# Optimization experiments

Measured on AMD Instinct MI355X. Metric: run time of the kernel, lower is better.

## Reference

```python
import jax, jax.numpy as jnp
import numpy as np
import math

B, S, D, H = 2048, 32, 1024, 16
DK = D // H
EPS = 1e-5

def setup_inputs() -> dict:
    key = jax.random.key(0)
    ks = jax.random.split(key, 8)
    w_scale = 0.02  # realistic init scale for linear weights
    # Weights stored as (d_in, d_out): y = x @ W + b (same math as torch x @ W.T)
    return {
        "x":  jax.random.normal(ks[0], (B, S, D), jnp.float32),
        "ln_g": jnp.ones((D,), jnp.float32),
        "ln_b": jnp.zeros((D,), jnp.float32),
        "wq": jax.random.normal(ks[1], (D, D), jnp.float32) * w_scale,
        "bq": jnp.zeros((D,), jnp.float32),
        "wk": jax.random.normal(ks[2], (D, D), jnp.float32) * w_scale,
        "bk": jnp.zeros((D,), jnp.float32),
        "wv": jax.random.normal(ks[3], (D, D), jnp.float32) * w_scale,
        "bv": jnp.zeros((D,), jnp.float32),
        "wo": jax.random.normal(ks[4], (D, D), jnp.float32) * w_scale,
        "bo": jnp.zeros((D,), jnp.float32),
        "rel_bias": jax.random.normal(ks[5], (H, 32, 32), jnp.float32),
    }

def reference(x, ln_g, ln_b, wq, bq, wk, bk, wv, bv, wo, bo, rel_bias):
    b, s, d = x.shape
    h = rel_bias.shape[0]
    dk = d // h
    residual = x
    # LayerNorm (eps=1e-5)
    mu = jnp.mean(x, axis=-1, keepdims=True)
    var = jnp.mean(jnp.square(x - mu), axis=-1, keepdims=True)
    xn = (x - mu) * jax.lax.rsqrt(var + EPS) * ln_g + ln_b
    # QKV projections -> [b, h, s, dk]
    def split_heads(t):
        return t.reshape(b, s, h, dk).transpose(0, 2, 1, 3)
    Q = split_heads(xn @ wq + bq)
    K = split_heads(xn @ wk + bk)
    V = split_heads(xn @ wv + bv)
    scores = jnp.einsum('bhqd,bhkd->bhqk', Q, K) / jnp.sqrt(jnp.float32(dk))
    if s <= 32:  # static at trace time, matching the torch branch
        scores = scores + rel_bias[:, :s, :s][None]
    attn = jax.nn.softmax(scores, axis=-1)
    ctx = jnp.einsum('bhqk,bhkd->bhqd', attn, V)
    ctx = ctx.transpose(0, 2, 1, 3).reshape(b, s, d)
    out = ctx @ wo + bo  # dropout is identity in eval
    return residual + out
```

## Files before the change

kernel.cpp:

```cpp
#include <hip/hip_runtime.h>
#include <stdint.h>


typedef __attribute__((ext_vector_type(8))) short bf16x8;
typedef __attribute__((ext_vector_type(4))) float f32x4;
typedef __attribute__((ext_vector_type(16))) float f32x16;

__device__ __forceinline__ float bf2f(unsigned short u) {
    return __uint_as_float(((unsigned)u) << 16);
}
__device__ __forceinline__ unsigned short f2bf(float f) {
    unsigned u = __float_as_uint(f);
    u += 0x7FFFu + ((u >> 16) & 1u);
    return (unsigned short)(u >> 16);
}
__device__ __forceinline__ uint4 pack8(const float* f) {
    uint4 u;
    u.x = (unsigned)f2bf(f[0]) | ((unsigned)f2bf(f[1]) << 16);
    u.y = (unsigned)f2bf(f[2]) | ((unsigned)f2bf(f[3]) << 16);
    u.z = (unsigned)f2bf(f[4]) | ((unsigned)f2bf(f[5]) << 16);
    u.w = (unsigned)f2bf(f[6]) | ((unsigned)f2bf(f[7]) << 16);
    return u;
}

typedef __attribute__((address_space(3))) unsigned lds_u32;
typedef const __attribute__((address_space(1))) unsigned glb_u32;
__device__ __forceinline__ void gld16(const void* g, void* l) {
    __builtin_amdgcn_global_load_lds((glb_u32*)g, (lds_u32*)l, 16, 0, 0);
}

__global__ __launch_bounds__(256) void transpose_w(
    const float* __restrict__ wq, const float* __restrict__ wk,
    const float* __restrict__ wv, const float* __restrict__ wo,
    unsigned short* __restrict__ wcatT, unsigned short* __restrict__ woT)
{
    __shared__ unsigned short T[64 * 72];
    int bid = blockIdx.x;
    int p = bid >> 8;
    int t = bid & 255;
    int k0 = (t >> 4) * 64, n0 = (t & 15) * 64;
    const float* src = (p == 0) ? wq : (p == 1) ? wk : (p == 2) ? wv : wo;
    unsigned short* dst = (p < 3) ? (wcatT + (size_t)p * 1048576) : woT;
    int tid = threadIdx.x;
#pragma unroll
    for (int it = 0; it < 2; it++) {
        int flat = it * 2048 + tid * 8;
        int r = flat >> 6, c = flat & 63;
        const float* s4 = src + (size_t)(k0 + r) * 1024 + n0 + c;
        float4 u0 = *(const float4*)s4;
        float4 u1 = *(const float4*)(s4 + 4);
        float f[8] = {u0.x, u0.y, u0.z, u0.w, u1.x, u1.y, u1.z, u1.w};
        *(uint4*)&T[r * 72 + c] = pack8(f);
    }
    __syncthreads();
#pragma unroll
    for (int it = 0; it < 2; it++) {
        int flat = it * 2048 + tid * 8;
        int rn = flat >> 6, ck = flat & 63;
        unsigned short v[8];
#pragma unroll
        for (int j = 0; j < 8; j++) v[j] = T[(ck + j) * 72 + rn];
        uint4 u;
        u.x = (unsigned)v[0] | ((unsigned)v[1] << 16);
        u.y = (unsigned)v[2] | ((unsigned)v[3] << 16);
        u.z = (unsigned)v[4] | ((unsigned)v[5] << 16);
        u.w = (unsigned)v[6] | ((unsigned)v[7] << 16);
        *(uint4*)(dst + (size_t)(n0 + rn) * 1024 + k0 + ck) = u;
    }
}

__global__ __launch_bounds__(256) void ln_kernel(
    const float* __restrict__ x, const float* __restrict__ gg,
    const float* __restrict__ bb, unsigned short* __restrict__ xn)
{
    int l = threadIdx.x & 63;
    size_t row = (size_t)blockIdx.x * 4 + (threadIdx.x >> 6);
    const float* xr = x + row * 1024;
    float f0[8], f1[8];
    *(float4*)&f0[0] = *(const float4*)(xr + l * 8);
    *(float4*)&f0[4] = *(const float4*)(xr + l * 8 + 4);
    *(float4*)&f1[0] = *(const float4*)(xr + 512 + l * 8);
    *(float4*)&f1[4] = *(const float4*)(xr + 512 + l * 8 + 4);
    float s = 0.f, s2 = 0.f;
#pragma unroll
    for (int j = 0; j < 8; j++) { s += f0[j] + f1[j]; s2 += f0[j] * f0[j] + f1[j] * f1[j]; }
#pragma unroll
    for (int m = 1; m < 64; m <<= 1) { s += __shfl_xor(s, m); s2 += __shfl_xor(s2, m); }
    float mu = s * (1.f / 1024.f);
    float var = s2 * (1.f / 1024.f) - mu * mu;
    float rs = rsqrtf(var + 1e-5f);
    float fg0[8], fg1[8], fb0[8], fb1[8];
    *(float4*)&fg0[0] = *(const float4*)(gg + l * 8);
    *(float4*)&fg0[4] = *(const float4*)(gg + l * 8 + 4);
    *(float4*)&fg1[0] = *(const float4*)(gg + 512 + l * 8);
    *(float4*)&fg1[4] = *(const float4*)(gg + 512 + l * 8 + 4);
    *(float4*)&fb0[0] = *(const float4*)(bb + l * 8);
    *(float4*)&fb0[4] = *(const float4*)(bb + l * 8 + 4);
    *(float4*)&fb1[0] = *(const float4*)(bb + 512 + l * 8);
    *(float4*)&fb1[4] = *(const float4*)(bb + 512 + l * 8 + 4);
    float o0[8], o1[8];
#pragma unroll
    for (int j = 0; j < 8; j++) {
        o0[j] = (f0[j] - mu) * rs * fg0[j] + fb0[j];
        o1[j] = (f1[j] - mu) * rs * fg1[j] + fb1[j];
    }
    *(uint4*)(xn + row * 1024 + l * 8) = pack8(o0);
    *(uint4*)(xn + row * 1024 + 512 + l * 8) = pack8(o1);
}

#define FENCE asm volatile("" ::: "memory")
#define BARRIER do { FENCE; __builtin_amdgcn_s_barrier(); FENCE; } while (0)
#define WAIT_LGKM0 do { asm volatile("s_waitcnt lgkmcnt(0)" ::: "memory"); \
                        __builtin_amdgcn_sched_barrier(0); } while (0)
#define VMCNT(n) asm volatile("s_waitcnt vmcnt(" #n ")" ::: "memory")

#define FQ_SA(buf) (LDSU + (buf) * 8192)
#define FQ_SB(buf) (LDSU + 16384 + (buf) * 12288)
#define QS_OFF 0
#define KS_OFF 9216
#define VT_OFF 18432
#define PS_OFF 28672

#define ASTG(buf, g, koff) gld16(Ag + (size_t)(g) * 32768 + (koff), \
                                 FQ_SA(buf) + ((g) * 32 + w * 8) * 64)
#define BSTG(buf, p, c, koff) gld16(((p) == 0 ? Bgq : (p) == 1 ? Bgk : Bgv) + (size_t)(c) * 32768 + (koff), \
                                    FQ_SB(buf) + ((p) * 64 + (c) * 32 + w * 8) * 64)

#define FLDA(buf, q, ks) (*(const bf16x8*)&FQ_SA(buf)[ \
    (wm * 64 + (q) * 16 + (l & 15)) * 64 + ((((ks) * 32) + khi) ^ aswz)])
#define FLDB(buf, cf, ks) (*(const bf16x8*)&FQ_SB(buf)[ \
    (wn * 96 + (cf) * 16 + (l & 15)) * 64 + ((((ks) * 32) + khi) ^ aswz)])

#define MFMA_HEX(q) do { \
    _Pragma("unroll") \
    for (int cf = 0; cf < 6; cf++) { \
        acc[q][cf] = __builtin_amdgcn_mfma_f32_16x16x32_bf16(aF0, bF[cf][0], acc[q][cf], 0, 0, 0); \
        acc[q][cf] = __builtin_amdgcn_mfma_f32_16x16x32_bf16(aF1, bF[cf][1], acc[q][cf], 0, 0, 0); \
    } } while (0)

#define FPHASE(buf, q, STAGE_STMT, TAIL_STMT) do { \
    bf16x8 aF0 = FLDA(buf, q, 0), aF1 = FLDA(buf, q, 1); \
    if ((q) == 0) { \
        _Pragma("unroll") \
        for (int cf = 0; cf < 6; cf++) { bF[cf][0] = FLDB(buf, cf, 0); bF[cf][1] = FLDB(buf, cf, 1); } \
    } \
    STAGE_STMT; \
    BARRIER; \
    WAIT_LGKM0; \
    __builtin_amdgcn_s_setprio(1); \
    MFMA_HEX(q); \
    __builtin_amdgcn_s_setprio(0); \
    TAIL_STMT; \
    BARRIER; \
} while (0)

__global__ __launch_bounds__(256, 2) void fqa2_kernel(
    const unsigned short* __restrict__ A, const unsigned short* __restrict__ wcatT,
    const float* __restrict__ bq, const float* __restrict__ bk,
    const float* __restrict__ bv, const float* __restrict__ rb,
    unsigned short* __restrict__ ctx)
{
    __shared__ __align__(16) unsigned short LDSU[40960];
    int cpx = gridDim.x >> 3;
    int bid = (blockIdx.x & 7) * cpx + (blockIdx.x >> 3);
    int mp = bid >> 4, h = bid & 15;
    int m0 = mp * 128;
    int tid = threadIdx.x, l = tid & 63, w = tid >> 6;
    int wm = w >> 1, wn = w & 1;
    int khi = (l >> 4) * 8;
    int aswz = (l & 7) * 8;
    int swzc = ((l & 7) ^ (l >> 3)) * 8;

    const unsigned short* Ag  = A + (size_t)(m0 + w * 8 + (l >> 3)) * 1024 + swzc;
    const unsigned short* Bgq = wcatT + (size_t)(h * 64 + w * 8 + (l >> 3)) * 1024 + swzc;
    const unsigned short* Bgk = Bgq + 1048576ull;
    const unsigned short* Bgv = Bgq + 2097152ull;

    f32x4 acc[4][6];
#pragma unroll
    for (int i = 0; i < 4; i++)
#pragma unroll
        for (int j = 0; j < 6; j++)
#pragma unroll
            for (int v = 0; v < 4; v++) acc[i][j][v] = 0.f;

    bf16x8 bF[6][2];

    ASTG(0, 0, 0); ASTG(0, 1, 0); ASTG(0, 2, 0); ASTG(0, 3, 0);
    BSTG(0, 0, 0, 0); BSTG(0, 0, 1, 0); BSTG(0, 1, 0, 0);
    BSTG(0, 1, 1, 0); BSTG(0, 2, 0, 0); BSTG(0, 2, 1, 0);
    BSTG(1, 0, 0, 64); BSTG(1, 0, 1, 64); BSTG(1, 1, 0, 64);
    BSTG(1, 1, 1, 64); BSTG(1, 2, 0, 64); BSTG(1, 2, 1, 64);
    VMCNT(6);
    BARRIER;

    for (int it = 0; it < 7; ++it) {
        int ko1 = (2 * it + 1) * 64, ko2 = (2 * it + 2) * 64, ko3 = (2 * it + 3) * 64;
        FPHASE(0, 0, do { ASTG(1, 0, ko1); ASTG(1, 1, ko1); } while (0), (void)0);
        FPHASE(0, 1, do { ASTG(1, 2, ko1); ASTG(1, 3, ko1); } while (0), (void)0);
        FPHASE(0, 2, do { BSTG(0, 0, 0, ko2); BSTG(0, 0, 1, ko2); BSTG(0, 1, 0, ko2); } while (0), (void)0);
        FPHASE(0, 3, do { BSTG(0, 1, 1, ko2); BSTG(0, 2, 0, ko2); BSTG(0, 2, 1, ko2); } while (0), VMCNT(6));
        FPHASE(1, 0, do { ASTG(0, 0, ko2); ASTG(0, 1, ko2); } while (0), (void)0);
        FPHASE(1, 1, do { ASTG(0, 2, ko2); ASTG(0, 3, ko2); } while (0), (void)0);
        FPHASE(1, 2, do { BSTG(1, 0, 0, ko3); BSTG(1, 0, 1, ko3); BSTG(1, 1, 0, ko3); } while (0), (void)0);
        FPHASE(1, 3, do { BSTG(1, 1, 1, ko3); BSTG(1, 2, 0, ko3); BSTG(1, 2, 1, ko3); } while (0), VMCNT(6));
    }
    FPHASE(0, 0, do { ASTG(1, 0, 960); ASTG(1, 1, 960); } while (0), (void)0);
    FPHASE(0, 1, do { ASTG(1, 2, 960); ASTG(1, 3, 960); } while (0), (void)0);
    FPHASE(0, 2, (void)0, (void)0);
    FPHASE(0, 3, (void)0, VMCNT(0));
    FPHASE(1, 0, (void)0, (void)0);
    FPHASE(1, 1, (void)0, (void)0);
    FPHASE(1, 2, (void)0, (void)0);
    FPHASE(1, 3, (void)0, (void)0);
    __builtin_amdgcn_sched_barrier(0);

#pragma unroll
    for (int cf = 0; cf < 6; cf++) {
        int colg = wn * 96 + cf * 16 + (l & 15);
        int seg = colg >> 6;
        int cseg = colg & 63;
        const float* bp = (seg == 0) ? bq : (seg == 1) ? bk : bv;
        float bias = bp[h * 64 + cseg];
#pragma unroll
        for (int ai = 0; ai < 4; ai++) {
#pragma unroll
            for (int v = 0; v < 4; v++) {
                int row = wm * 64 + ai * 16 + (l >> 4) * 4 + v;
                unsigned short val = f2bf(acc[ai][cf][v] + bias);
                if (seg == 0)      LDSU[QS_OFF + row * 72 + cseg] = val;
                else if (seg == 1) LDSU[KS_OFF + row * 72 + cseg] = val;
                else               LDSU[VT_OFF + (((row >> 5) << 6) + cseg) * 40 + (row & 31)] = val;
            }
        }
    }
    __syncthreads();

    {
        int col = l & 31, hi = l >> 5;
        f32x16 s;
#pragma unroll
        for (int i = 0; i < 16; i++) s[i] = 0.f;
#pragma unroll
        for (int t = 0; t < 4; t++) {
            bf16x8 aQ = *(const bf16x8*)&LDSU[QS_OFF + (w * 32 + col) * 72 + t * 16 + hi * 8];
            bf16x8 bK = *(const bf16x8*)&LDSU[KS_OFF + (w * 32 + col) * 72 + t * 16 + hi * 8];
            s = __builtin_amdgcn_mfma_f32_32x32x16_bf16(aQ, bK, s, 0, 0, 0);
        }
        const float* rbh = rb + h * 1024;
        unsigned short* ps = LDSU + PS_OFF + w * 1280;
#pragma unroll
        for (int r = 0; r < 16; r++) {
            int m = (r & 3) + 8 * (r >> 2) + 4 * hi;
            float v = s[r] * 0.125f + rbh[m * 32 + col];
            float mx = v;
#pragma unroll
            for (int msk = 1; msk < 32; msk <<= 1) mx = fmaxf(mx, __shfl_xor(mx, msk));
            float e = __expf(v - mx);
            float sm = e;
#pragma unroll
            for (int msk = 1; msk < 32; msk <<= 1) sm += __shfl_xor(sm, msk);
            ps[m * 40 + col] = f2bf(e / sm);
        }
        bf16x8 pa0 = *(const bf16x8*)&ps[col * 40 + hi * 8];
        bf16x8 pa1 = *(const bf16x8*)&ps[col * 40 + 16 + hi * 8];
        size_t rowb = ((size_t)mp * 4 + w) * 32;
#pragma unroll
        for (int c2 = 0; c2 < 2; c2++) {
            bf16x8 vb0 = *(const bf16x8*)&LDSU[VT_OFF + (w * 64 + c2 * 32 + col) * 40 + hi * 8];
            bf16x8 vb1 = *(const bf16x8*)&LDSU[VT_OFF + (w * 64 + c2 * 32 + col) * 40 + 16 + hi * 8];
            f32x16 o;
#pragma unroll
            for (int i = 0; i < 16; i++) o[i] = 0.f;
            o = __builtin_amdgcn_mfma_f32_32x32x16_bf16(pa0, vb0, o, 0, 0, 0);
            o = __builtin_amdgcn_mfma_f32_32x32x16_bf16(pa1, vb1, o, 0, 0, 0);
#pragma unroll
            for (int r = 0; r < 16; r++) {
                int m = (r & 3) + 8 * (r >> 2) + 4 * hi;
                ctx[(rowb + m) * 1024 + h * 64 + c2 * 32 + col] = f2bf(o[r]);
            }
        }
    }
}

#define SAp(buf) (LDSB + (buf) * 16384)
#define SBp(buf) (LDSB + 32768 + (buf) * 16384)

#define STG(gb, hh, kcol, ldsreg) do { \
    const unsigned short* _g = (gb) + (size_t)((hh) * 128) * 1024 + (kcol); \
    unsigned short* _d = (ldsreg) + ((hh) * 128 + w * 8) * 64; \
    gld16(_g, _d); gld16(_g + 64 * 1024, _d + 64 * 64); } while (0)

#define LDA(buf, q, rfq, ks) (*(const bf16x8*)&SAp(buf)[ \
    (wm * 128 + (q) * 32 + (rfq) * 16 + (l & 15)) * 64 + ((((ks) * 32) + khi) ^ aswz)])
#define LDB(buf, cf, ks) (*(const bf16x8*)&SBp(buf)[ \
    (wn * 64 + (cf) * 16 + (l & 15)) * 64 + ((((ks) * 32) + khi) ^ aswz)])

#define MFMA_QUAD(q) do { \
    _Pragma("unroll") \
    for (int cf = 0; cf < 4; cf++) { \
        acc[(q)*2+0][cf] = __builtin_amdgcn_mfma_f32_16x16x32_bf16(aF00, bF[cf][0], acc[(q)*2+0][cf], 0, 0, 0); \
        acc[(q)*2+0][cf] = __builtin_amdgcn_mfma_f32_16x16x32_bf16(aF01, bF[cf][1], acc[(q)*2+0][cf], 0, 0, 0); \
        acc[(q)*2+1][cf] = __builtin_amdgcn_mfma_f32_16x16x32_bf16(aF10, bF[cf][0], acc[(q)*2+1][cf], 0, 0, 0); \
        acc[(q)*2+1][cf] = __builtin_amdgcn_mfma_f32_16x16x32_bf16(aF11, bF[cf][1], acc[(q)*2+1][cf], 0, 0, 0); \
    } } while (0)

#define PHASE(buf, q, STAGE_STMT, TAIL_STMT) do { \
    bf16x8 aF00 = LDA(buf, q, 0, 0), aF01 = LDA(buf, q, 0, 1); \
    bf16x8 aF10 = LDA(buf, q, 1, 0), aF11 = LDA(buf, q, 1, 1); \
    if ((q) == 0) { \
        _Pragma("unroll") \
        for (int cf = 0; cf < 4; cf++) { bF[cf][0] = LDB(buf, cf, 0); bF[cf][1] = LDB(buf, cf, 1); } \
    } \
    STAGE_STMT; \
    BARRIER; \
    WAIT_LGKM0; \
    __builtin_amdgcn_s_setprio(1); \
    MFMA_QUAD(q); \
    __builtin_amdgcn_s_setprio(0); \
    TAIL_STMT; \
    BARRIER; \
} while (0)

__global__ __launch_bounds__(512, 2) void gemm8res(
    const unsigned short* __restrict__ A, const unsigned short* __restrict__ Bt,
    const float* __restrict__ bz0, const float* __restrict__ resid,
    float* __restrict__ out, int NTL)
{
    __shared__ __align__(16) unsigned short LDSB[65536];
    int cpx = gridDim.x >> 3;
    int bid = (blockIdx.x & 7) * cpx + (blockIdx.x >> 3);
    int mt = bid / NTL, ntl = bid % NTL;
    int m0 = mt * 256, n0 = ntl * 256;
    int tid = threadIdx.x, l = tid & 63, w = tid >> 6;
    int wm = w >> 2, wn = w & 3;
    int khi = (l >> 4) * 8;
    int aswz = (l & 7) * 8;

    const unsigned short* Ag = A + (size_t)(m0 + w * 8 + (l >> 3)) * 1024 + ((l & 7) ^ (l >> 3)) * 8;
    const unsigned short* Bg = Bt + (size_t)(n0 + w * 8 + (l >> 3)) * 1024 + ((l & 7) ^ (l >> 3)) * 8;
    unsigned short* sA0 = SAp(0);
    unsigned short* sA1 = SAp(1);
    unsigned short* sB0 = SBp(0);
    unsigned short* sB1 = SBp(1);

    f32x4 acc[8][4];
#pragma unroll
    for (int i = 0; i < 8; i++)
#pragma unroll
        for (int j = 0; j < 4; j++)
#pragma unroll
            for (int v = 0; v < 4; v++) acc[i][j][v] = 0.f;

    bf16x8 bF[4][2];

    STG(Ag, 0, 0, sA0); STG(Ag, 1, 0, sA0);
    STG(Bg, 0, 0, sB0); STG(Bg, 1, 0, sB0);
    STG(Bg, 0, 64, sB1); STG(Bg, 1, 64, sB1);
    VMCNT(4);
    BARRIER;

    for (int it = 0; it < 7; ++it) {
        int koff = it * 128;
        PHASE(0, 0, STG(Ag, 0, koff + 64, sA1), (void)0);
        PHASE(0, 1, STG(Ag, 1, koff + 64, sA1), (void)0);
        PHASE(0, 2, STG(Bg, 0, koff + 128, sB0), (void)0);
        PHASE(0, 3, STG(Bg, 1, koff + 128, sB0), VMCNT(4));
        PHASE(1, 0, STG(Ag, 0, koff + 128, sA0), (void)0);
        PHASE(1, 1, STG(Ag, 1, koff + 128, sA0), (void)0);
        PHASE(1, 2, STG(Bg, 0, koff + 192, sB1), (void)0);
        PHASE(1, 3, STG(Bg, 1, koff + 192, sB1), VMCNT(4));
    }
    PHASE(0, 0, STG(Ag, 0, 960, sA1), (void)0);
    PHASE(0, 1, STG(Ag, 1, 960, sA1), (void)0);
    PHASE(0, 2, (void)0, (void)0);
    PHASE(0, 3, (void)0, VMCNT(0));
    PHASE(1, 0, (void)0, (void)0);
    PHASE(1, 1, (void)0, (void)0);
    PHASE(1, 2, (void)0, (void)0);
    PHASE(1, 3, (void)0, (void)0);
    __builtin_amdgcn_sched_barrier(0);

    float* Cf = (float*)LDSB;
    int gcol = n0 + l * 4;
    float4 bzv = *(const float4*)(bz0 + gcol);
#pragma unroll
    for (int pass = 0; pass < 2; pass++) {
        __syncthreads();
#pragma unroll
        for (int rfq = 0; rfq < 4; rfq++) {
            int rf = pass * 4 + rfq;
#pragma unroll
            for (int cf = 0; cf < 4; cf++) {
                int c0 = wn * 64 + cf * 16 + (l & 15);
                int c4 = c0 >> 2, ce = c0 & 3;
#pragma unroll
                for (int v = 0; v < 4; v++) {
                    int rl = wm * 64 + rfq * 16 + (l >> 4) * 4 + v;
                    Cf[rl * 256 + ((c4 ^ (rl & 7)) << 2) + ce] = acc[rf][cf][v];
                }
            }
        }
        __syncthreads();
#pragma unroll
        for (int rb4 = 0; rb4 < 4; rb4++) {
            float4 rz[4], cv[4];
#pragma unroll
            for (int k = 0; k < 4; k++) {
                int rr = (rb4 * 4 + k) * 8 + w;
                int grow = m0 + (rr & 63) + ((rr >> 6) << 7) + pass * 64;
                rz[k] = *(const float4*)(resid + (size_t)grow * 1024 + gcol);
            }
#pragma unroll
            for (int k = 0; k < 4; k++) {
                int rr = (rb4 * 4 + k) * 8 + w;
                cv[k] = *(const float4*)&Cf[rr * 256 + ((l ^ (rr & 7)) << 2)];
            }
#pragma unroll
            for (int k = 0; k < 4; k++) {
                int rr = (rb4 * 4 + k) * 8 + w;
                int grow = m0 + (rr & 63) + ((rr >> 6) << 7) + pass * 64;
                float4 o;
                o.x = cv[k].x + bzv.x + rz[k].x;
                o.y = cv[k].y + bzv.y + rz[k].y;
                o.z = cv[k].z + bzv.z + rz[k].z;
                o.w = cv[k].w + bzv.w + rz[k].w;
                *(float4*)(out + (size_t)grow * 1024 + gcol) = o;
            }
        }
    }
}

extern "C" void kernel_launch(void* const* d_in, const int* in_sizes, int n_in,
                              void* d_out, int out_size, void* d_ws, size_t ws_size,
                              hipStream_t stream)
{
    const float* x  = (const float*)d_in[0];
    const float* lg = (const float*)d_in[1];
    const float* lb = (const float*)d_in[2];
    const float* wq = (const float*)d_in[3];
    const float* bq = (const float*)d_in[4];
    const float* wk = (const float*)d_in[5];
    const float* bk = (const float*)d_in[6];
    const float* wv = (const float*)d_in[7];
    const float* bv = (const float*)d_in[8];
    const float* wo = (const float*)d_in[9];
    const float* bo = (const float*)d_in[10];
    const float* rb = (const float*)d_in[11];
    float* out = (float*)d_out;
    unsigned short* ws = (unsigned short*)d_ws;

    unsigned short* wcatT = ws;
    unsigned short* woT   = wcatT + 3145728;
    unsigned short* xn    = woT + 1048576;
    unsigned short* ctx   = xn + 67108864ull;

    transpose_w<<<dim3(1024), dim3(256), 0, stream>>>(wq, wk, wv, wo, wcatT, woT);
    ln_kernel<<<dim3(16384), dim3(256), 0, stream>>>(x, lg, lb, xn);

    fqa2_kernel<<<dim3(8192), dim3(256), 0, stream>>>(xn, wcatT, bq, bk, bv, rb, ctx);

    gemm8res<<<dim3(1024), dim3(512), 0, stream>>>(ctx, woT, bo, x, out, 4);
}
```

Measured before the change: 777.8 us.

## Merge LN and weight transpose launches, loop heads per block, batch residual loads

Merges the weight transpose and LayerNorm into one launch, with extra blocks handling the transpose. The fused QKV+attention kernel now runs 512 blocks, each looping over all 16 heads, instead of 8192 blocks with one head each. This is meant to reuse the A tile through cache and cut launch/tail overhead, but it reduces parallelism to 512 blocks on a 256-CU device. The output GEMM epilogue now prefetches 16 residual rows into registers before each repack, which raises register pressure.

```diff
diff --git a/kernel.cpp b/kernel.cpp
--- a/kernel.cpp
+++ b/kernel.cpp
@@ -29,50 +29,49 @@
     __builtin_amdgcn_global_load_lds((glb_u32*)g, (lds_u32*)l, 16, 0, 0);
 }
 
-__global__ __launch_bounds__(256) void transpose_w(
+__global__ __launch_bounds__(256) void lnw_kernel(
+    const float* __restrict__ x, const float* __restrict__ gg,
+    const float* __restrict__ bb, unsigned short* __restrict__ xn,
     const float* __restrict__ wq, const float* __restrict__ wk,
     const float* __restrict__ wv, const float* __restrict__ wo,
     unsigned short* __restrict__ wcatT, unsigned short* __restrict__ woT)
 {
     __shared__ unsigned short T[64 * 72];
-    int bid = blockIdx.x;
-    int p = bid >> 8;
-    int t = bid & 255;
-    int k0 = (t >> 4) * 64, n0 = (t & 15) * 64;
-    const float* src = (p == 0) ? wq : (p == 1) ? wk : (p == 2) ? wv : wo;
-    unsigned short* dst = (p < 3) ? (wcatT + (size_t)p * 1048576) : woT;
-    int tid = threadIdx.x;
-#pragma unroll
-    for (int it = 0; it < 2; it++) {
-        int flat = it * 2048 + tid * 8;
-        int r = flat >> 6, c = flat & 63;
-        const float* s4 = src + (size_t)(k0 + r) * 1024 + n0 + c;
-        float4 u0 = *(const float4*)s4;
-        float4 u1 = *(const float4*)(s4 + 4);
-        float f[8] = {u0.x, u0.y, u0.z, u0.w, u1.x, u1.y, u1.z, u1.w};
-        *(uint4*)&T[r * 72 + c] = pack8(f);
-    }
-    __syncthreads();
-#pragma unroll
-    for (int it = 0; it < 2; it++) {
-        int flat = it * 2048 + tid * 8;
-        int rn = flat >> 6, ck = flat & 63;
-        unsigned short v[8];
-#pragma unroll
-        for (int j = 0; j < 8; j++) v[j] = T[(ck + j) * 72 + rn];
-        uint4 u;
-        u.x = (unsigned)v[0] | ((unsigned)v[1] << 16);
-        u.y = (unsigned)v[2] | ((unsigned)v[3] << 16);
-        u.z = (unsigned)v[4] | ((unsigned)v[5] << 16);
-        u.w = (unsigned)v[6] | ((unsigned)v[7] << 16);
-        *(uint4*)(dst + (size_t)(n0 + rn) * 1024 + k0 + ck) = u;
-    }
-}
-
-__global__ __launch_bounds__(256) void ln_kernel(
-    const float* __restrict__ x, const float* __restrict__ gg,
-    const float* __restrict__ bb, unsigned short* __restrict__ xn)
-{
+    if (blockIdx.x >= 16384) {
+        int bid = blockIdx.x - 16384;
+        int p = bid >> 8;
+        int t = bid & 255;
+        int k0 = (t >> 4) * 64, n0 = (t & 15) * 64;
+        const float* src = (p == 0) ? wq : (p == 1) ? wk : (p == 2) ? wv : wo;
+        unsigned short* dst = (p < 3) ? (wcatT + (size_t)p * 1048576) : woT;
+        int tid = threadIdx.x;
+#pragma unroll
+        for (int it = 0; it < 2; it++) {
+            int flat = it * 2048 + tid * 8;
+            int r = flat >> 6, c = flat & 63;
+            const float* s4 = src + (size_t)(k0 + r) * 1024 + n0 + c;
+            float4 u0 = *(const float4*)s4;
+            float4 u1 = *(const float4*)(s4 + 4);
+            float f[8] = {u0.x, u0.y, u0.z, u0.w, u1.x, u1.y, u1.z, u1.w};
+            *(uint4*)&T[r * 72 + c] = pack8(f);
+        }
+        __syncthreads();
+#pragma unroll
+        for (int it = 0; it < 2; it++) {
+            int flat = it * 2048 + tid * 8;
+            int rn = flat >> 6, ck = flat & 63;
+            unsigned short v[8];
+#pragma unroll
+            for (int j = 0; j < 8; j++) v[j] = T[(ck + j) * 72 + rn];
+            uint4 u;
+            u.x = (unsigned)v[0] | ((unsigned)v[1] << 16);
+            u.y = (unsigned)v[2] | ((unsigned)v[3] << 16);
+            u.z = (unsigned)v[4] | ((unsigned)v[5] << 16);
+            u.w = (unsigned)v[6] | ((unsigned)v[7] << 16);
+            *(uint4*)(dst + (size_t)(n0 + rn) * 1024 + k0 + ck) = u;
+        }
+        return;
+    }
     int l = threadIdx.x & 63;
     size_t row = (size_t)blockIdx.x * 4 + (threadIdx.x >> 6);
     const float* xr = x + row * 1024;
@@ -154,7 +153,7 @@
     BARRIER; \
 } while (0)
 
-__global__ __launch_bounds__(256, 2) void fqa2_kernel(
+__global__ __launch_bounds__(256, 2) void fqa3_kernel(
     const unsigned short* __restrict__ A, const unsigned short* __restrict__ wcatT,
     const float* __restrict__ bq, const float* __restrict__ bk,
     const float* __restrict__ bv, const float* __restrict__ rb,
@@ -163,7 +162,7 @@
     __shared__ __align__(16) unsigned short LDSU[40960];
     int cpx = gridDim.x >> 3;
     int bid = (blockIdx.x & 7) * cpx + (blockIdx.x >> 3);
-    int mp = bid >> 4, h = bid & 15;
+    int mp = bid;
     int m0 = mp * 128;
     int tid = threadIdx.x, l = tid & 63, w = tid >> 6;
     int wm = w >> 1, wn = w & 1;
@@ -171,115 +170,120 @@
     int aswz = (l & 7) * 8;
     int swzc = ((l & 7) ^ (l >> 3)) * 8;
 
-    const unsigned short* Ag  = A + (size_t)(m0 + w * 8 + (l >> 3)) * 1024 + swzc;
-    const unsigned short* Bgq = wcatT + (size_t)(h * 64 + w * 8 + (l >> 3)) * 1024 + swzc;
-    const unsigned short* Bgk = Bgq + 1048576ull;
-    const unsigned short* Bgv = Bgq + 2097152ull;
-
-    f32x4 acc[4][6];
-#pragma unroll
-    for (int i = 0; i < 4; i++)
-#pragma unroll
-        for (int j = 0; j < 6; j++)
-#pragma unroll
-            for (int v = 0; v < 4; v++) acc[i][j][v] = 0.f;
-
-    bf16x8 bF[6][2];
-
-    ASTG(0, 0, 0); ASTG(0, 1, 0); ASTG(0, 2, 0); ASTG(0, 3, 0);
-    BSTG(0, 0, 0, 0); BSTG(0, 0, 1, 0); BSTG(0, 1, 0, 0);
-    BSTG(0, 1, 1, 0); BSTG(0, 2, 0, 0); BSTG(0, 2, 1, 0);
-    BSTG(1, 0, 0, 64); BSTG(1, 0, 1, 64); BSTG(1, 1, 0, 64);
-    BSTG(1, 1, 1, 64); BSTG(1, 2, 0, 64); BSTG(1, 2, 1, 64);
-    VMCNT(6);
-    BARRIER;
-
-    for (int it = 0; it < 7; ++it) {
-        int ko1 = (2 * it + 1) * 64, ko2 = (2 * it + 2) * 64, ko3 = (2 * it + 3) * 64;
-        FPHASE(0, 0, do { ASTG(1, 0, ko1); ASTG(1, 1, ko1); } while (0), (void)0);
-        FPHASE(0, 1, do { ASTG(1, 2, ko1); ASTG(1, 3, ko1); } while (0), (void)0);
-        FPHASE(0, 2, do { BSTG(0, 0, 0, ko2); BSTG(0, 0, 1, ko2); BSTG(0, 1, 0, ko2); } while (0), (void)0);
-        FPHASE(0, 3, do { BSTG(0, 1, 1, ko2); BSTG(0, 2, 0, ko2); BSTG(0, 2, 1, ko2); } while (0), VMCNT(6));
-        FPHASE(1, 0, do { ASTG(0, 0, ko2); ASTG(0, 1, ko2); } while (0), (void)0);
-        FPHASE(1, 1, do { ASTG(0, 2, ko2); ASTG(0, 3, ko2); } while (0), (void)0);
-        FPHASE(1, 2, do { BSTG(1, 0, 0, ko3); BSTG(1, 0, 1, ko3); BSTG(1, 1, 0, ko3); } while (0), (void)0);
-        FPHASE(1, 3, do { BSTG(1, 1, 1, ko3); BSTG(1, 2, 0, ko3); BSTG(1, 2, 1, ko3); } while (0), VMCNT(6));
-    }
-    FPHASE(0, 0, do { ASTG(1, 0, 960); ASTG(1, 1, 960); } while (0), (void)0);
-    FPHASE(0, 1, do { ASTG(1, 2, 960); ASTG(1, 3, 960); } while (0), (void)0);
-    FPHASE(0, 2, (void)0, (void)0);
-    FPHASE(0, 3, (void)0, VMCNT(0));
-    FPHASE(1, 0, (void)0, (void)0);
-    FPHASE(1, 1, (void)0, (void)0);
-    FPHASE(1, 2, (void)0, (void)0);
-    FPHASE(1, 3, (void)0, (void)0);
-    __builtin_amdgcn_sched_barrier(0);
-
-#pragma unroll
-    for (int cf = 0; cf < 6; cf++) {
-        int colg = wn * 96 + cf * 16 + (l & 15);
-        int seg = colg >> 6;
-        int cseg = colg & 63;
-        const float* bp = (seg == 0) ? bq : (seg == 1) ? bk : bv;
-        float bias = bp[h * 64 + cseg];
-#pragma unroll
-        for (int ai = 0; ai < 4; ai++) {
-#pragma unroll
-            for (int v = 0; v < 4; v++) {
-                int row = wm * 64 + ai * 16 + (l >> 4) * 4 + v;
-                unsigned short val = f2bf(acc[ai][cf][v] + bias);
-                if (seg == 0)      LDSU[QS_OFF + row * 72 + cseg] = val;
-                else if (seg == 1) LDSU[KS_OFF + row * 72 + cseg] = val;
-                else               LDSU[VT_OFF + (((row >> 5) << 6) + cseg) * 40 + (row & 31)] = val;
+    const unsigned short* Ag = A + (size_t)(m0 + w * 8 + (l >> 3)) * 1024 + swzc;
+
+#pragma unroll 1
+    for (int h = 0; h < 16; ++h) {
+        const unsigned short* Bgq = wcatT + (size_t)(h * 64 + w * 8 + (l >> 3)) * 1024 + swzc;
+        const unsigned short* Bgk = Bgq + 1048576ull;
+        const unsigned short* Bgv = Bgq + 2097152ull;
+
+        f32x4 acc[4][6];
+#pragma unroll
+        for (int i = 0; i < 4; i++)
+#pragma unroll
+            for (int j = 0; j < 6; j++)
+#pragma unroll
+                for (int v = 0; v < 4; v++) acc[i][j][v] = 0.f;
+
+        bf16x8 bF[6][2];
+
+        ASTG(0, 0, 0); ASTG(0, 1, 0); ASTG(0, 2, 0); ASTG(0, 3, 0);
+        BSTG(0, 0, 0, 0); BSTG(0, 0, 1, 0); BSTG(0, 1, 0, 0);
+        BSTG(0, 1, 1, 0); BSTG(0, 2, 0, 0); BSTG(0, 2, 1, 0);
+        BSTG(1, 0, 0, 64); BSTG(1, 0, 1, 64); BSTG(1, 1, 0, 64);
+        BSTG(1, 1, 1, 64); BSTG(1, 2, 0, 64); BSTG(1, 2, 1, 64);
+        VMCNT(6);
+        BARRIER;
+
+        for (int it = 0; it < 7; ++it) {
+            int ko1 = (2 * it + 1) * 64, ko2 = (2 * it + 2) * 64, ko3 = (2 * it + 3) * 64;
+            FPHASE(0, 0, do { ASTG(1, 0, ko1); ASTG(1, 1, ko1); } while (0), (void)0);
+            FPHASE(0, 1, do { ASTG(1, 2, ko1); ASTG(1, 3, ko1); } while (0), (void)0);
+            FPHASE(0, 2, do { BSTG(0, 0, 0, ko2); BSTG(0, 0, 1, ko2); BSTG(0, 1, 0, ko2); } while (0), (void)0);
+            FPHASE(0, 3, do { BSTG(0, 1, 1, ko2); BSTG(0, 2, 0, ko2); BSTG(0, 2, 1, ko2); } while (0), VMCNT(6));
+            FPHASE(1, 0, do { ASTG(0, 0, ko2); ASTG(0, 1, ko2); } while (0), (void)0);
+            FPHASE(1, 1, do { ASTG(0, 2, ko2); ASTG(0, 3, ko2); } while (0), (void)0);
+            FPHASE(1, 2, do { BSTG(1, 0, 0, ko3); BSTG(1, 0, 1, ko3); BSTG(1, 1, 0, ko3); } while (0), (void)0);
+            FPHASE(1, 3, do { BSTG(1, 1, 1, ko3); BSTG(1, 2, 0, ko3); BSTG(1, 2, 1, ko3); } while (0), VMCNT(6));
+        }
+        FPHASE(0, 0, do { ASTG(1, 0, 960); ASTG(1, 1, 960); } while (0), (void)0);
+        FPHASE(0, 1, do { ASTG(1, 2, 960); ASTG(1, 3, 960); } while (0), (void)0);
+        FPHASE(0, 2, (void)0, (void)0);
+        FPHASE(0, 3, (void)0, VMCNT(0));
+        FPHASE(1, 0, (void)0, (void)0);
+        FPHASE(1, 1, (void)0, (void)0);
+        FPHASE(1, 2, (void)0, (void)0);
+        FPHASE(1, 3, (void)0, (void)0);
+        __builtin_amdgcn_sched_barrier(0);
+
+#pragma unroll
+        for (int cf = 0; cf < 6; cf++) {
+            int colg = wn * 96 + cf * 16 + (l & 15);
+            int seg = colg >> 6;
+            int cseg = colg & 63;
+            const float* bp = (seg == 0) ? bq : (seg == 1) ? bk : bv;
+            float bias = bp[h * 64 + cseg];
+#pragma unroll
+            for (int ai = 0; ai < 4; ai++) {
+#pragma unroll
+                for (int v = 0; v < 4; v++) {
+                    int row = wm * 64 + ai * 16 + (l >> 4) * 4 + v;
+                    unsigned short val = f2bf(acc[ai][cf][v] + bias);
+                    if (seg == 0)      LDSU[QS_OFF + row * 72 + cseg] = val;
+                    else if (seg == 1) LDSU[KS_OFF + row * 72 + cseg] = val;
+                    else               LDSU[VT_OFF + (((row >> 5) << 6) + cseg) * 40 + (row & 31)] = val;
+                }
             }
         }
-    }
-    __syncthreads();
-
-    {
-        int col = l & 31, hi = l >> 5;
-        f32x16 s;
-#pragma unroll
-        for (int i = 0; i < 16; i++) s[i] = 0.f;
-#pragma unroll
-        for (int t = 0; t < 4; t++) {
-            bf16x8 aQ = *(const bf16x8*)&LDSU[QS_OFF + (w * 32 + col) * 72 + t * 16 + hi * 8];
-            bf16x8 bK = *(const bf16x8*)&LDSU[KS_OFF + (w * 32 + col) * 72 + t * 16 + hi * 8];
-            s = __builtin_amdgcn_mfma_f32_32x32x16_bf16(aQ, bK, s, 0, 0, 0);
-        }
-        const float* rbh = rb + h * 1024;
-        unsigned short* ps = LDSU + PS_OFF + w * 1280;
-#pragma unroll
-        for (int r = 0; r < 16; r++) {
-            int m = (r & 3) + 8 * (r >> 2) + 4 * hi;
-            float v = s[r] * 0.125f + rbh[m * 32 + col];
-            float mx = v;
-#pragma unroll
-            for (int msk = 1; msk < 32; msk <<= 1) mx = fmaxf(mx, __shfl_xor(mx, msk));
-            float e = __expf(v - mx);
-            float sm = e;
-#pragma unroll
-            for (int msk = 1; msk < 32; msk <<= 1) sm += __shfl_xor(sm, msk);
-            ps[m * 40 + col] = f2bf(e / sm);
-        }
-        bf16x8 pa0 = *(const bf16x8*)&ps[col * 40 + hi * 8];
-        bf16x8 pa1 = *(const bf16x8*)&ps[col * 40 + 16 + hi * 8];
-        size_t rowb = ((size_t)mp * 4 + w) * 32;
-#pragma unroll
-        for (int c2 = 0; c2 < 2; c2++) {
-            bf16x8 vb0 = *(const bf16x8*)&LDSU[VT_OFF + (w * 64 + c2 * 32 + col) * 40 + hi * 8];
-            bf16x8 vb1 = *(const bf16x8*)&LDSU[VT_OFF + (w * 64 + c2 * 32 + col) * 40 + 16 + hi * 8];
-            f32x16 o;
-#pragma unroll
-            for (int i = 0; i < 16; i++) o[i] = 0.f;
-            o = __builtin_amdgcn_mfma_f32_32x32x16_bf16(pa0, vb0, o, 0, 0, 0);
-            o = __builtin_amdgcn_mfma_f32_32x32x16_bf16(pa1, vb1, o, 0, 0, 0);
+        __syncthreads();
+
+        {
+            int col = l & 31, hi = l >> 5;
+            f32x16 s;
+#pragma unroll
+            for (int i = 0; i < 16; i++) s[i] = 0.f;
+#pragma unroll
+            for (int t = 0; t < 4; t++) {
+                bf16x8 aQ = *(const bf16x8*)&LDSU[QS_OFF + (w * 32 + col) * 72 + t * 16 + hi * 8];
+                bf16x8 bK = *(const bf16x8*)&LDSU[KS_OFF + (w * 32 + col) * 72 + t * 16 + hi * 8];
+                s = __builtin_amdgcn_mfma_f32_32x32x16_bf16(aQ, bK, s, 0, 0, 0);
+            }
+            const float* rbh = rb + h * 1024;
+            unsigned short* ps = LDSU + PS_OFF + w * 1280;
 #pragma unroll
             for (int r = 0; r < 16; r++) {
                 int m = (r & 3) + 8 * (r >> 2) + 4 * hi;
-                ctx[(rowb + m) * 1024 + h * 64 + c2 * 32 + col] = f2bf(o[r]);
+                float v = s[r] * 0.125f + rbh[m * 32 + col];
+                float mx = v;
+#pragma unroll
+                for (int msk = 1; msk < 32; msk <<= 1) mx = fmaxf(mx, __shfl_xor(mx, msk));
+                float e = __expf(v - mx);
+                float sm = e;
+#pragma unroll
+                for (int msk = 1; msk < 32; msk <<= 1) sm += __shfl_xor(sm, msk);
+                ps[m * 40 + col] = f2bf(e / sm);
+            }
+            bf16x8 pa0 = *(const bf16x8*)&ps[col * 40 + hi * 8];
+            bf16x8 pa1 = *(const bf16x8*)&ps[col * 40 + 16 + hi * 8];
+            size_t rowb = ((size_t)mp * 4 + w) * 32;
+#pragma unroll
+            for (int c2 = 0; c2 < 2; c2++) {
+                bf16x8 vb0 = *(const bf16x8*)&LDSU[VT_OFF + (w * 64 + c2 * 32 + col) * 40 + hi * 8];
+                bf16x8 vb1 = *(const bf16x8*)&LDSU[VT_OFF + (w * 64 + c2 * 32 + col) * 40 + 16 + hi * 8];
+                f32x16 o;
+#pragma unroll
+                for (int i = 0; i < 16; i++) o[i] = 0.f;
+                o = __builtin_amdgcn_mfma_f32_32x32x16_bf16(pa0, vb0, o, 0, 0, 0);
+                o = __builtin_amdgcn_mfma_f32_32x32x16_bf16(pa1, vb1, o, 0, 0, 0);
+#pragma unroll
+                for (int r = 0; r < 16; r++) {
+                    int m = (r & 3) + 8 * (r >> 2) + 4 * hi;
+                    ctx[(rowb + m) * 1024 + h * 64 + c2 * 32 + col] = f2bf(o[r]);
+                }
             }
         }
+        __syncthreads();
     }
 }
 
@@ -322,6 +326,22 @@
     BARRIER; \
 } while (0)
 
+#define REPACK(pass) do { \
+    _Pragma("unroll") \
+    for (int rfq = 0; rfq < 4; rfq++) { \
+        int rf = (pass) * 4 + rfq; \
+        _Pragma("unroll") \
+        for (int cf = 0; cf < 4; cf++) { \
+            int c0 = wn * 64 + cf * 16 + (l & 15); \
+            int c4 = c0 >> 2, ce = c0 & 3; \
+            _Pragma("unroll") \
+            for (int v = 0; v < 4; v++) { \
+                int rl = wm * 64 + rfq * 16 + (l >> 4) * 4 + v; \
+                Cf[rl * 256 + ((c4 ^ (rl & 7)) << 2) + ce] = acc[rf][cf][v]; \
+            } \
+        } \
+    } } while (0)
+
 __global__ __launch_bounds__(512, 2) void gemm8res(
     const unsigned short* __restrict__ A, const unsigned short* __restrict__ Bt,
     const float* __restrict__ bz0, const float* __restrict__ resid,
@@ -384,50 +404,49 @@
     float* Cf = (float*)LDSB;
     int gcol = n0 + l * 4;
     float4 bzv = *(const float4*)(bz0 + gcol);
-#pragma unroll
-    for (int pass = 0; pass < 2; pass++) {
-        __syncthreads();
-#pragma unroll
-        for (int rfq = 0; rfq < 4; rfq++) {
-            int rf = pass * 4 + rfq;
-#pragma unroll
-            for (int cf = 0; cf < 4; cf++) {
-                int c0 = wn * 64 + cf * 16 + (l & 15);
-                int c4 = c0 >> 2, ce = c0 & 3;
-#pragma unroll
-                for (int v = 0; v < 4; v++) {
-                    int rl = wm * 64 + rfq * 16 + (l >> 4) * 4 + v;
-                    Cf[rl * 256 + ((c4 ^ (rl & 7)) << 2) + ce] = acc[rf][cf][v];
-                }
-            }
-        }
-        __syncthreads();
-#pragma unroll
-        for (int rb4 = 0; rb4 < 4; rb4++) {
-            float4 rz[4], cv[4];
-#pragma unroll
-            for (int k = 0; k < 4; k++) {
-                int rr = (rb4 * 4 + k) * 8 + w;
-                int grow = m0 + (rr & 63) + ((rr >> 6) << 7) + pass * 64;
-                rz[k] = *(const float4*)(resid + (size_t)grow * 1024 + gcol);
-            }
-#pragma unroll
-            for (int k = 0; k < 4; k++) {
-                int rr = (rb4 * 4 + k) * 8 + w;
-                cv[k] = *(const float4*)&Cf[rr * 256 + ((l ^ (rr & 7)) << 2)];
-            }
-#pragma unroll
-            for (int k = 0; k < 4; k++) {
-                int rr = (rb4 * 4 + k) * 8 + w;
-                int grow = m0 + (rr & 63) + ((rr >> 6) << 7) + pass * 64;
-                float4 o;
-                o.x = cv[k].x + bzv.x + rz[k].x;
-                o.y = cv[k].y + bzv.y + rz[k].y;
-                o.z = cv[k].z + bzv.z + rz[k].z;
-                o.w = cv[k].w + bzv.w + rz[k].w;
-                *(float4*)(out + (size_t)grow * 1024 + gcol) = o;
-            }
-        }
+
+    float4 rzp[16];
+#pragma unroll
+    for (int k = 0; k < 16; k++) {
+        int rr = k * 8 + w;
+        int grow = m0 + (rr & 63) + ((rr >> 6) << 7);
+        rzp[k] = *(const float4*)(resid + (size_t)grow * 1024 + gcol);
+    }
+    __syncthreads();
+    REPACK(0);
+    __syncthreads();
+#pragma unroll
+    for (int k = 0; k < 16; k++) {
+        int rr = k * 8 + w;
+        int grow = m0 + (rr & 63) + ((rr >> 6) << 7);
+        float4 cv = *(const float4*)&Cf[rr * 256 + ((l ^ (rr & 7)) << 2)];
+        float4 o;
+        o.x = cv.x + bzv.x + rzp[k].x;
+        o.y = cv.y + bzv.y + rzp[k].y;
+        o.z = cv.z + bzv.z + rzp[k].z;
+        o.w = cv.w + bzv.w + rzp[k].w;
+        *(float4*)(out + (size_t)grow * 1024 + gcol) = o;
+    }
+#pragma unroll
+    for (int k = 0; k < 16; k++) {
+        int rr = k * 8 + w;
+        int grow = m0 + (rr & 63) + ((rr >> 6) << 7) + 64;
+        rzp[k] = *(const float4*)(resid + (size_t)grow * 1024 + gcol);
+    }
+    __syncthreads();
+    REPACK(1);
+    __syncthreads();
+#pragma unroll
+    for (int k = 0; k < 16; k++) {
+        int rr = k * 8 + w;
+        int grow = m0 + (rr & 63) + ((rr >> 6) << 7) + 64;
+        float4 cv = *(const float4*)&Cf[rr * 256 + ((l ^ (rr & 7)) << 2)];
+        float4 o;
+        o.x = cv.x + bzv.x + rzp[k].x;
+        o.y = cv.y + bzv.y + rzp[k].y;
+        o.z = cv.z + bzv.z + rzp[k].z;
+        o.w = cv.w + bzv.w + rzp[k].w;
+        *(float4*)(out + (size_t)grow * 1024 + gcol) = o;
     }
 }
 
@@ -455,10 +474,10 @@
     unsigned short* xn    = woT + 1048576;
     unsigned short* ctx   = xn + 67108864ull;
 
-    transpose_w<<<dim3(1024), dim3(256), 0, stream>>>(wq, wk, wv, wo, wcatT, woT);
-    ln_kernel<<<dim3(16384), dim3(256), 0, stream>>>(x, lg, lb, xn);
-
-    fqa2_kernel<<<dim3(8192), dim3(256), 0, stream>>>(xn, wcatT, bq, bk, bv, rb, ctx);
+    lnw_kernel<<<dim3(17408), dim3(256), 0, stream>>>(
+        x, lg, lb, xn, wq, wk, wv, wo, wcatT, woT);
+
+    fqa3_kernel<<<dim3(512), dim3(256), 0, stream>>>(xn, wcatT, bq, bk, bv, rb, ctx);
 
     gemm8res<<<dim3(1024), dim3(512), 0, stream>>>(ctx, woT, bo, x, out, 4);
 }
```

Result: slower. 1.365 ms (+75.5%).
